# Kernel tuning notes

Measured on AMD Instinct MI355X. Metric: run time of the kernel, lower is better.

The kernel has to match this reference:

```python
import jax, jax.numpy as jnp
import numpy as np

LATENT = 1024
HID = 512
J = 24
# SMPL kinematic tree (parent[0] = -1 is the root, unused in the loop)
PARENT = [-1, 0, 0, 0, 1, 2, 3, 4, 5, 6, 7, 8, 9, 9, 9, 12, 13, 14, 16, 17, 18, 19, 20, 21]
EPS = 1e-12  # F.normalize default eps


def setup_inputs() -> dict:
    key = jax.random.key(0)
    k1, k2, k3, k4, k5 = jax.random.split(key, 5)
    B = 32768
    # Kaiming-uniform-ish init scales for the Linear layers
    s1 = 1.0 / np.sqrt(LATENT)
    s2 = 1.0 / np.sqrt(HID)
    return {
        "z": jax.random.normal(k1, (B, LATENT), dtype=jnp.float32),
        "W1": jax.random.uniform(k2, (LATENT, HID), minval=-s1, maxval=s1, dtype=jnp.float32),
        "b1": jax.random.uniform(k3, (HID,), minval=-s1, maxval=s1, dtype=jnp.float32),
        "W2": jax.random.uniform(k4, (HID, (J - 1) * 4), minval=-s2, maxval=s2, dtype=jnp.float32),
        "b2": jax.random.uniform(k5, ((J - 1) * 4,), minval=-s2, maxval=s2, dtype=jnp.float32),
    }


def reference(z, W1, b1, W2, b2):
    B = z.shape[0]
    h = jax.nn.silu(z @ W1 + b1)                    # [B, 512]
    raw = (h @ W2 + b2).reshape(B, J - 1, 4)        # [B, J-1, 4]
    vec = raw[..., :3]                              # [B, J-1, 3]
    norm = jnp.linalg.norm(vec, axis=-1, keepdims=True)
    direction = vec / jnp.maximum(norm, EPS)        # F.normalize(dim=-1)
    length = jax.nn.softplus(raw[..., 3])           # [B, J-1]
    child_off = direction * length[..., None]       # [B, J-1, 3]
    offsets = jnp.concatenate(
        [jnp.zeros((B, 1, 3), dtype=z.dtype), child_off], axis=1
    )                                                # [B, J, 3]
    # Static-tree forward kinematics: unroll the (small, fixed) joint loop.
    joints_list = [jnp.zeros((B, 3), dtype=z.dtype)]
    for j in range(1, J):
        joints_list.append(joints_list[PARENT[j]] + offsets[:, j])
    joints = jnp.stack(joints_list, axis=1)          # [B, J, 3]
    return (joints, offsets, length)
```

## Files before the change

kernel.cpp:

```cpp
#include <hip/hip_runtime.h>
#include <hip/hip_bf16.h>
#include <stdint.h>

#define BROWS 32768
#define LATENT 1024
#define HID 512

typedef float f32x4 __attribute__((ext_vector_type(4)));
typedef __bf16 bf16x8 __attribute__((ext_vector_type(8)));
typedef unsigned short us8 __attribute__((ext_vector_type(8)));

__device__ __forceinline__ void gload16(const void* g, void* l) {
  __builtin_amdgcn_global_load_lds(
      (__attribute__((address_space(1))) void*)g,
      (__attribute__((address_space(3))) void*)l, 16, 0, 0);
}

__device__ __forceinline__ void split_bf16(float x, unsigned short& hi, unsigned short& lo) {
  __bf16 h = (__bf16)x;
  float r = x - (float)h;
  __bf16 l = (__bf16)r;
  hi = __builtin_bit_cast(unsigned short, h);
  lo = __builtin_bit_cast(unsigned short, l);
}

__device__ __forceinline__ f32x4 mfma16(bf16x8 a, bf16x8 b, f32x4 c) {
  return __builtin_amdgcn_mfma_f32_16x16x32_bf16(a, b, c, 0, 0, 0);
}

__device__ __forceinline__ bf16x8 ldfrag(const void* p) {
  return __builtin_bit_cast(bf16x8, *(const us8*)p);
}

__global__ __launch_bounds__(256) void k_prep_w1f(const float* __restrict__ W1,
                                                  unsigned short* __restrict__ w1f) {
  const int n = blockIdx.x;
  const int t = threadIdx.x;
  const int kt = t >> 3, ls = t & 7;
  const int p = ls ^ (n & 7);
  const int k0 = kt * 32 + (ls & 3) * 8;
  unsigned short v[8];
#pragma unroll
  for (int e = 0; e < 8; e++) {
    const float x = W1[(size_t)(k0 + e) * HID + n];
    unsigned short h, q;
    split_bf16(x, h, q);
    v[e] = (ls < 4) ? h : q;
  }
  unsigned short* dst = w1f + ((size_t)n * 32 + kt) * 64 + p * 8;
  *(ushort4*)(dst) = make_ushort4(v[0], v[1], v[2], v[3]);
  *(ushort4*)(dst + 4) = make_ushort4(v[4], v[5], v[6], v[7]);
}

__global__ __launch_bounds__(256) void k_prep_w2t(const float* __restrict__ W2,
                                                  unsigned short* __restrict__ hi,
                                                  unsigned short* __restrict__ lo) {
  const int idx = blockIdx.x * 256 + threadIdx.x;
  const int n = idx >> 9, k = idx & 511;
  const float v = (n < 92) ? W2[(size_t)k * 92 + n] : 0.0f;
  unsigned short h, l;
  split_bf16(v, h, l);
  hi[idx] = h;
  lo[idx] = l;
}

__global__ __launch_bounds__(256, 2) void k_gemm1(
    const float* __restrict__ z, const unsigned short* __restrict__ w1f,
    const float* __restrict__ b1,
    unsigned short* __restrict__ hh, unsigned short* __restrict__ hl) {
  extern __shared__ __align__(16) char lb[];

  const int tid = threadIdx.x;
  const int bid = blockIdx.x;
  const int swz = (bid & 7) * 64 + (bid >> 3);
  const int mb = swz >> 1, nbk = swz & 1;
  const int m0 = mb * 128, n0g = nbk * 256;

  const int wv = tid >> 6, l = tid & 63;
  const int wr = wv >> 1, wc = wv & 1;
  const int l15 = l & 15, lg = l >> 4;
  const int xr = l15 & 7;

  const int bhB = (wc * 128 + l15) * 128 + ((lg ^ xr) << 4);
  const int blB = (wc * 128 + l15) * 128 + ((((4 | lg) ^ xr)) << 4);

  const float* zb = z + (size_t)(m0 + wr * 64 + l15) * LATENT + lg * 8;

  const unsigned short* bsrc =
      w1f + ((size_t)(n0g + wv * 64 + (l >> 3)) * 32) * 64 + (l & 7) * 8;

  f32x4 acc[4][8] = {};
  float4 arl[4], arh[4];
  bf16x8 ah[4], alo[4];

#define LOAD_A(kt1)                                                           \
  {                                                                           \
    _Pragma("unroll") for (int mf = 0; mf < 4; mf++) {                        \
      const float* p_ = zb + (size_t)(16 * mf) * LATENT + (kt1) * 32;         \
      arl[mf] = *(const float4*)(p_);                                         \
      arh[mf] = *(const float4*)(p_ + 4);                                     \
    }                                                                         \
  }

#define SPLIT_A                                                               \
  {                                                                           \
    _Pragma("unroll") for (int mf = 0; mf < 4; mf++) {                        \
      _Pragma("unroll") for (int e = 0; e < 4; e++) {                         \
        float f0 = arl[mf][e], f1 = arh[mf][e];                               \
        __bf16 h0 = (__bf16)f0, h1 = (__bf16)f1;                              \
        ah[mf][e] = h0;     alo[mf][e] = (__bf16)(f0 - (float)h0);            \
        ah[mf][4 + e] = h1; alo[mf][4 + e] = (__bf16)(f1 - (float)h1);        \
      }                                                                       \
    }                                                                         \
  }

#define GLOAD_B(bufo, kt1)                                                    \
  {                                                                           \
    _Pragma("unroll") for (int j_ = 0; j_ < 8; j_++)                          \
        gload16(bsrc + (size_t)j_ * 16384 + (kt1) * 64,                       \
                lb + (bufo) + (wv * 64 + j_ * 8) * 128);                      \
  }

#define COMPUTE(bufo)                                                         \
  {                                                                           \
    __builtin_amdgcn_s_setprio(1);                                            \
    _Pragma("unroll") for (int nf = 0; nf < 8; nf++) {                        \
      bf16x8 bh = ldfrag(lb + (bufo) + bhB + nf * 2048);                      \
      _Pragma("unroll") for (int mf = 0; mf < 4; mf++)                        \
          acc[mf][nf] = mfma16(ah[mf], bh, acc[mf][nf]);                      \
      _Pragma("unroll") for (int mf = 0; mf < 4; mf++)                        \
          acc[mf][nf] = mfma16(alo[mf], bh, acc[mf][nf]);                     \
    }                                                                         \
    _Pragma("unroll") for (int nf = 0; nf < 8; nf++) {                        \
      bf16x8 bl = ldfrag(lb + (bufo) + blB + nf * 2048);                      \
      _Pragma("unroll") for (int mf = 0; mf < 4; mf++)                        \
          acc[mf][nf] = mfma16(ah[mf], bl, acc[mf][nf]);                      \
    }                                                                         \
    __builtin_amdgcn_s_setprio(0);                                            \
  }

  GLOAD_B(0, 0);
  LOAD_A(0);

#pragma unroll 2
  for (int t = 0; t < 32; ++t) {
    const int cb = (t & 1) * 32768;
    const int nb2 = cb ^ 32768;

    asm volatile("s_waitcnt vmcnt(8)" ::: "memory");
    __builtin_amdgcn_s_barrier();

    if (t < 31) {
      GLOAD_B(nb2, t + 1);
      asm volatile("s_waitcnt vmcnt(8)" ::: "memory");
    } else {
      asm volatile("s_waitcnt vmcnt(0)" ::: "memory");
    }
    SPLIT_A;
    if (t < 31) LOAD_A(t + 1);

    COMPUTE(cb);
  }

  float b1v[8];
#pragma unroll
  for (int nf = 0; nf < 8; nf++) b1v[nf] = b1[n0g + wc * 128 + nf * 16 + l15];

#pragma unroll
  for (int mf = 0; mf < 4; mf++)
#pragma unroll
    for (int nf = 0; nf < 8; nf++)
#pragma unroll
      for (int r = 0; r < 4; r++) {
        const int gm = m0 + wr * 64 + mf * 16 + (lg << 2) + r;
        const int gn = n0g + wc * 128 + nf * 16 + l15;
        const float x = acc[mf][nf][r] + b1v[nf];
        const float hval = x / (1.0f + expf(-x));
        unsigned short hi_, lo_;
        split_bf16(hval, hi_, lo_);
        const size_t o = (size_t)gm * HID + gn;
        hh[o] = hi_;
        hl[o] = lo_;
      }
}

__global__ __launch_bounds__(256, 2) void k_gemm2(
    const unsigned short* __restrict__ hh, const unsigned short* __restrict__ hl,
    const unsigned short* __restrict__ w2h, const unsigned short* __restrict__ w2l,
    const float* __restrict__ b2, float* __restrict__ out) {
  __shared__ unsigned short Ah[2][2048], Al[2][2048];
  __shared__ unsigned short Bh[2][4096], Bl[2][4096];
  __shared__ float raw[64][97];

  const int tid = threadIdx.x;
  const int m0 = blockIdx.x * 64;
  const int w = tid >> 6, lane = tid & 63;
  const int wr = w >> 1, wc = w & 1;
  const int l15 = lane & 15, lg = lane >> 4;
  const int arow = tid >> 2, ac8 = (tid & 3) << 3;

  const unsigned short* hhb = hh + (size_t)(m0 + arow) * HID + ac8;
  const unsigned short* hlb = hl + (size_t)(m0 + arow) * HID + ac8;
  const unsigned short* w2hb = w2h + (size_t)arow * HID + ac8;
  const unsigned short* w2lb = w2l + (size_t)arow * HID + ac8;

  f32x4 acc[2][3] = {};

#define G2_STAGE(kt, bf) { \
    gload16(hhb + (kt) * 32, &Ah[bf][(w << 9)]); \
    gload16(hlb + (kt) * 32, &Al[bf][(w << 9)]); \
    gload16(w2hb + (kt) * 32,            &Bh[bf][(w << 9)]); \
    gload16(w2hb + (kt) * 32 + 64 * HID, &Bh[bf][2048 + (w << 9)]); \
    gload16(w2lb + (kt) * 32,            &Bl[bf][(w << 9)]); \
    gload16(w2lb + (kt) * 32 + 64 * HID, &Bl[bf][2048 + (w << 9)]); }

#define G2_COMPUTE(bf) { \
    bf16x8 ah2[2], al2[2], bh2[3], bl2[3]; \
    _Pragma("unroll") \
    for (int mf = 0; mf < 2; mf++) { \
      const int o_ = ((wr * 32 + mf * 16 + l15) << 5) + (lg << 3); \
      ah2[mf] = ldfrag(&Ah[bf][o_]); \
      al2[mf] = ldfrag(&Al[bf][o_]); \
    } \
    _Pragma("unroll") \
    for (int nf = 0; nf < 3; nf++) { \
      const int o_ = ((wc * 48 + nf * 16 + l15) << 5) + (lg << 3); \
      bh2[nf] = ldfrag(&Bh[bf][o_]); \
      bl2[nf] = ldfrag(&Bl[bf][o_]); \
    } \
    _Pragma("unroll") \
    for (int mf = 0; mf < 2; mf++) { \
      _Pragma("unroll") \
      for (int nf = 0; nf < 3; nf++) { \
        acc[mf][nf] = mfma16(ah2[mf], bh2[nf], acc[mf][nf]); \
        acc[mf][nf] = mfma16(al2[mf], bh2[nf], acc[mf][nf]); \
        acc[mf][nf] = mfma16(ah2[mf], bl2[nf], acc[mf][nf]); \
      } } }

  G2_STAGE(0, 0);
  __syncthreads();
#pragma unroll 2
  for (int kt = 0; kt < 16; kt++) {
    const int cur = kt & 1, nx = cur ^ 1;
    if (kt < 15) G2_STAGE(kt + 1, nx);
    G2_COMPUTE(cur);
    __syncthreads();
  }

#pragma unroll
  for (int mf = 0; mf < 2; mf++) {
#pragma unroll
    for (int nf = 0; nf < 3; nf++) {
#pragma unroll
      for (int r = 0; r < 4; r++) {
        const int ml = wr * 32 + mf * 16 + (lg << 2) + r;
        const int nl = wc * 48 + nf * 16 + l15;
        raw[ml][nl] = acc[mf][nf][r];
      }
    }
  }
  __syncthreads();

  const size_t OFFB = (size_t)BROWS * 72;
  const size_t LENB = (size_t)BROWS * 144;

  for (int task = tid; task < 64 * 24; task += 256) {
    const int row = task / 24;
    const int j = task - row * 24;
    const int gm = m0 + row;
    float* orow = out + OFFB + (size_t)gm * 72;
    if (j == 0) {
      orow[0] = 0.0f; orow[1] = 0.0f; orow[2] = 0.0f;
    } else {
      const int c0 = (j - 1) * 4;
      const float vx = raw[row][c0 + 0] + b2[c0 + 0];
      const float vy = raw[row][c0 + 1] + b2[c0 + 1];
      const float vz = raw[row][c0 + 2] + b2[c0 + 2];
      const float wvv = raw[row][c0 + 3] + b2[c0 + 3];
      const float nrm = sqrtf(vx * vx + vy * vy + vz * vz);
      const float inv = 1.0f / fmaxf(nrm, 1e-12f);
      const float len = fmaxf(wvv, 0.0f) + log1pf(expf(-fabsf(wvv)));
      const float sc = inv * len;
      const float ox = vx * sc, oy = vy * sc, oz = vz * sc;
      orow[j * 3 + 0] = ox; orow[j * 3 + 1] = oy; orow[j * 3 + 2] = oz;
      out[LENB + (size_t)gm * 23 + (j - 1)] = len;
      raw[row][c0 + 0] = ox; raw[row][c0 + 1] = oy; raw[row][c0 + 2] = oz;
    }
  }
  __syncthreads();

  if (tid < 64) {
    constexpr int PAR[24] = {-1, 0, 0, 0, 1, 2, 3, 4, 5, 6, 7, 8,
                             9, 9, 9, 12, 13, 14, 16, 17, 18, 19, 20, 21};
    const int gm = m0 + tid;
    float e[72];
    e[0] = 0.0f; e[1] = 0.0f; e[2] = 0.0f;
#pragma unroll
    for (int j = 1; j < 24; j++) {
      const int p = PAR[j];
      const int c0 = (j - 1) * 4;
      e[3 * j + 0] = e[3 * p + 0] + raw[tid][c0 + 0];
      e[3 * j + 1] = e[3 * p + 1] + raw[tid][c0 + 1];
      e[3 * j + 2] = e[3 * p + 2] + raw[tid][c0 + 2];
    }
    float4* jo = (float4*)(out + (size_t)gm * 72);
#pragma unroll
    for (int q = 0; q < 18; q++)
      jo[q] = make_float4(e[4 * q + 0], e[4 * q + 1], e[4 * q + 2], e[4 * q + 3]);
  }
}

extern "C" void kernel_launch(void* const* d_in, const int* in_sizes, int n_in,
                              void* d_out, int out_size, void* d_ws, size_t ws_size,
                              hipStream_t stream) {
  const float* z = (const float*)d_in[0];
  const float* W1 = (const float*)d_in[1];
  const float* b1 = (const float*)d_in[2];
  const float* W2 = (const float*)d_in[3];
  const float* b2 = (const float*)d_in[4];
  float* out = (float*)d_out;

  char* ws = (char*)d_ws;
  unsigned short* w1f = (unsigned short*)(ws);
  unsigned short* w2h = (unsigned short*)(ws + (2 << 20));
  unsigned short* w2l = (unsigned short*)(ws + (2 << 20) + 131072);
  unsigned short* hh = (unsigned short*)(ws + ((size_t)4 << 20));
  unsigned short* hl = (unsigned short*)(ws + ((size_t)4 << 20) + ((size_t)32 << 20));

  hipFuncSetAttribute((const void*)k_gemm1,
                      hipFuncAttributeMaxDynamicSharedMemorySize, 131072);

  hipLaunchKernelGGL(k_prep_w1f, dim3(512), dim3(256), 0, stream, W1, w1f);
  hipLaunchKernelGGL(k_prep_w2t, dim3(256), dim3(256), 0, stream, W2, w2h, w2l);
  hipLaunchKernelGGL(k_gemm1, dim3(512), dim3(256), 65536, stream, z, w1f, b1, hh, hl);
  hipLaunchKernelGGL(k_gemm2, dim3(512), dim3(256), 0, stream, hh, hl, w2h, w2l, b2, out);
}
```

Before: 147.8 us.

## Shrink GEMM1 to single-wave 64x64 tiles without block barriers

Restructures the first GEMM from 256-thread blocks computing 128x256 tiles into single-wave 64-thread blocks computing 64x64 tiles, launched as 4096 blocks with static 32KB LDS. Because each block is one wave, the workgroup barrier is dropped and only vmcnt waits order the double-buffered LDS loads. The goal is to remove barrier stalls and raise occupancy and scheduling flexibility. The cost is far less reuse: each z row tile is reloaded and re-split by 8 column blocks instead of 2, and each W1 tile is fetched by many more blocks, which raises global and L2 traffic.

```diff
diff --git a/kernel.cpp b/kernel.cpp
--- a/kernel.cpp
+++ b/kernel.cpp
@@ -64,32 +64,30 @@
   lo[idx] = l;
 }
 
-__global__ __launch_bounds__(256, 2) void k_gemm1(
+__global__ __launch_bounds__(64, 3) void k_gemm1(
     const float* __restrict__ z, const unsigned short* __restrict__ w1f,
     const float* __restrict__ b1,
     unsigned short* __restrict__ hh, unsigned short* __restrict__ hl) {
-  extern __shared__ __align__(16) char lb[];
-
-  const int tid = threadIdx.x;
+  __shared__ __attribute__((aligned(16))) char lb[32768];
+
   const int bid = blockIdx.x;
-  const int swz = (bid & 7) * 64 + (bid >> 3);
-  const int mb = swz >> 1, nbk = swz & 1;
-  const int m0 = mb * 128, n0g = nbk * 256;
-
-  const int wv = tid >> 6, l = tid & 63;
-  const int wr = wv >> 1, wc = wv & 1;
+  const int swz = (bid & 7) * 512 + (bid >> 3);
+  const int mb = swz >> 3, nbk = swz & 7;
+  const int m0 = mb * 64, n0g = nbk * 64;
+
+  const int l = threadIdx.x;
   const int l15 = l & 15, lg = l >> 4;
   const int xr = l15 & 7;
 
-  const int bhB = (wc * 128 + l15) * 128 + ((lg ^ xr) << 4);
-  const int blB = (wc * 128 + l15) * 128 + ((((4 | lg) ^ xr)) << 4);
-
-  const float* zb = z + (size_t)(m0 + wr * 64 + l15) * LATENT + lg * 8;
+  const int bhB = l15 * 128 + ((lg ^ xr) << 4);
+  const int blB = l15 * 128 + ((((4 | lg) ^ xr)) << 4);
+
+  const float* zb = z + (size_t)(m0 + l15) * LATENT + lg * 8;
 
   const unsigned short* bsrc =
-      w1f + ((size_t)(n0g + wv * 64 + (l >> 3)) * 32) * 64 + (l & 7) * 8;
-
-  f32x4 acc[4][8] = {};
+      w1f + ((size_t)(n0g + (l >> 3)) * 32) * 64 + (l & 7) * 8;
+
+  f32x4 acc[4][4] = {};
   float4 arl[4], arh[4];
   bf16x8 ah[4], alo[4];
 
@@ -118,20 +116,20 @@
   {                                                                           \
     _Pragma("unroll") for (int j_ = 0; j_ < 8; j_++)                          \
         gload16(bsrc + (size_t)j_ * 16384 + (kt1) * 64,                       \
-                lb + (bufo) + (wv * 64 + j_ * 8) * 128);                      \
+                lb + (bufo) + j_ * 1024);                                     \
   }
 
 #define COMPUTE(bufo)                                                         \
   {                                                                           \
     __builtin_amdgcn_s_setprio(1);                                            \
-    _Pragma("unroll") for (int nf = 0; nf < 8; nf++) {                        \
+    _Pragma("unroll") for (int nf = 0; nf < 4; nf++) {                        \
       bf16x8 bh = ldfrag(lb + (bufo) + bhB + nf * 2048);                      \
       _Pragma("unroll") for (int mf = 0; mf < 4; mf++)                        \
           acc[mf][nf] = mfma16(ah[mf], bh, acc[mf][nf]);                      \
       _Pragma("unroll") for (int mf = 0; mf < 4; mf++)                        \
           acc[mf][nf] = mfma16(alo[mf], bh, acc[mf][nf]);                     \
     }                                                                         \
-    _Pragma("unroll") for (int nf = 0; nf < 8; nf++) {                        \
+    _Pragma("unroll") for (int nf = 0; nf < 4; nf++) {                        \
       bf16x8 bl = ldfrag(lb + (bufo) + blB + nf * 2048);                      \
       _Pragma("unroll") for (int mf = 0; mf < 4; mf++)                        \
           acc[mf][nf] = mfma16(ah[mf], bl, acc[mf][nf]);                      \
@@ -139,41 +137,38 @@
     __builtin_amdgcn_s_setprio(0);                                            \
   }
 
+#define FENCE asm volatile("" ::: "memory")
+
   GLOAD_B(0, 0);
+  FENCE;
   LOAD_A(0);
 
-#pragma unroll 2
   for (int t = 0; t < 32; ++t) {
-    const int cb = (t & 1) * 32768;
-    const int nb2 = cb ^ 32768;
+    const int cb = (t & 1) << 13;
+    const int nx = cb ^ 8192;
 
     asm volatile("s_waitcnt vmcnt(8)" ::: "memory");
-    __builtin_amdgcn_s_barrier();
-
     if (t < 31) {
-      GLOAD_B(nb2, t + 1);
-      asm volatile("s_waitcnt vmcnt(8)" ::: "memory");
-    } else {
-      asm volatile("s_waitcnt vmcnt(0)" ::: "memory");
+      GLOAD_B(nx, t + 1);
+      FENCE;
     }
     SPLIT_A;
     if (t < 31) LOAD_A(t + 1);
-
     COMPUTE(cb);
   }
 
-  float b1v[8];
-#pragma unroll
-  for (int nf = 0; nf < 8; nf++) b1v[nf] = b1[n0g + wc * 128 + nf * 16 + l15];
+  float b1v[4];
+#pragma unroll
+  for (int nf = 0; nf < 4; nf++) b1v[nf] = b1[n0g + nf * 16 + l15];
 
 #pragma unroll
   for (int mf = 0; mf < 4; mf++)
 #pragma unroll
-    for (int nf = 0; nf < 8; nf++)
+    for (int nf = 0; nf < 4; nf++)
 #pragma unroll
       for (int r = 0; r < 4; r++) {
-        const int gm = m0 + wr * 64 + mf * 16 + (lg << 2) + r;
-        const int gn = n0g + wc * 128 + nf * 16 + l15;
+        const int gm = m0 + mf * 16 + (lg << 2) + r;
+        const int gn = n0g + nf * 16 + l15;
         const float x = acc[mf][nf][r] + b1v[nf];
         const float hval = x / (1.0f + expf(-x));
         unsigned short hi_, lo_;
@@ -327,11 +322,8 @@
   unsigned short* hh = (unsigned short*)(ws + ((size_t)4 << 20));
   unsigned short* hl = (unsigned short*)(ws + ((size_t)4 << 20) + ((size_t)32 << 20));
 
-  hipFuncSetAttribute((const void*)k_gemm1,
-                      hipFuncAttributeMaxDynamicSharedMemorySize, 131072);
-
   hipLaunchKernelGGL(k_prep_w1f, dim3(512), dim3(256), 0, stream, W1, w1f);
   hipLaunchKernelGGL(k_prep_w2t, dim3(256), dim3(256), 0, stream, W2, w2h, w2l);
-  hipLaunchKernelGGL(k_gemm1, dim3(512), dim3(256), 65536, stream, z, w1f, b1, hh, hl);
+  hipLaunchKernelGGL(k_gemm1, dim3(4096), dim3(64), 0, stream, z, w1f, b1, hh, hl);
   hipLaunchKernelGGL(k_gemm2, dim3(512), dim3(256), 0, stream, hh, hl, w2h, w2l, b2, out);
 }
```

Result: slower. 244.3 us (+65.2%).

## Restructure GEMM1 to 8 waves with LDS-staged A tiles and phased MFMA pipeline

Applied to the files above, without the earlier changes.

GEMM1 moves from 4 to 8 waves per block, each wave computing a 64x64 sub-tile instead of 64x128. The fp32 z tile is now staged into LDS through async global-to-LDS loads, replacing direct register loads, and shares a double buffer with the B tile. The main loop splits into three MFMA phases (hi*hi, lo*hi, hi*lo) with barriers between them so fragment loads and prefetch can overlap compute. This lowers per-wave register pressure and raises latency hiding, at the cost of more barriers and more LDS (96KB per block), which may limit occupancy.

```diff
diff --git a/kernel.cpp b/kernel.cpp
--- a/kernel.cpp
+++ b/kernel.cpp
@@ -64,7 +64,7 @@
   lo[idx] = l;
 }
 
-__global__ __launch_bounds__(256, 2) void k_gemm1(
+__global__ __launch_bounds__(512, 2) void k_gemm1(
     const float* __restrict__ z, const unsigned short* __restrict__ w1f,
     const float* __restrict__ b1,
     unsigned short* __restrict__ hh, unsigned short* __restrict__ hl) {
@@ -77,103 +77,132 @@
   const int m0 = mb * 128, n0g = nbk * 256;
 
   const int wv = tid >> 6, l = tid & 63;
-  const int wr = wv >> 1, wc = wv & 1;
+  const int wr = wv >> 2, wc = wv & 3;
   const int l15 = l & 15, lg = l >> 4;
-  const int xr = l15 & 7;
-
-  const int bhB = (wc * 128 + l15) * 128 + ((lg ^ xr) << 4);
-  const int blB = (wc * 128 + l15) * 128 + ((((4 | lg) ^ xr)) << 4);
-
-  const float* zb = z + (size_t)(m0 + wr * 64 + l15) * LATENT + lg * 8;
-
-  const unsigned short* bsrc =
-      w1f + ((size_t)(n0g + wv * 64 + (l >> 3)) * 32) * 64 + (l & 7) * 8;
-
-  f32x4 acc[4][8] = {};
-  float4 arl[4], arh[4];
-  bf16x8 ah[4], alo[4];
-
-#define LOAD_A(kt1)                                                           \
+  const int x7 = l15 & 7;
+
+  const int rowAB = (wr * 64 + l15) * 128;
+  const int sA0 = (((2 * lg) ^ x7)) << 4;
+  const int sA1 = (((2 * lg + 1) ^ x7)) << 4;
+  const int rowBB = 16384 + (wc * 64 + l15) * 128;
+  const int sBH = ((lg ^ x7)) << 4;
+  const int sBL = ((((4 | lg)) ^ x7)) << 4;
+
+  const int lr = l >> 3, lc = l & 7;
+  const char* zA0 = (const char*)z +
+      ((size_t)(m0 + wv * 16 + lr)) * 4096 + ((lc ^ (lr & 7)) << 4);
+  const char* zB0 = (const char*)w1f +
+      ((size_t)(n0g + wv * 32 + lr)) * 4096 + (lc << 4);
+
+  f32x4 acc[4][4] = {};
+  f32x4 af[4][2];
+  bf16x8 ah[4], al[4], bhf[4], blf[4];
+
+#define STAGE(nbase, kt1)                                                     \
+  {                                                                           \
+    _Pragma("unroll") for (int j_ = 0; j_ < 2; j_++)                          \
+        gload16(zA0 + (size_t)j_ * 32768 + (kt1) * 128,                       \
+                lb + (nbase) + (wv * 2 + j_) * 1024);                         \
+    _Pragma("unroll") for (int j_ = 0; j_ < 4; j_++)                          \
+        gload16(zB0 + (size_t)j_ * 32768 + (kt1) * 128,                       \
+                lb + (nbase) + 16384 + (wv * 4 + j_) * 1024);                 \
+  }
+
+#define LD_A(cb)                                                              \
   {                                                                           \
     _Pragma("unroll") for (int mf = 0; mf < 4; mf++) {                        \
-      const float* p_ = zb + (size_t)(16 * mf) * LATENT + (kt1) * 32;         \
-      arl[mf] = *(const float4*)(p_);                                         \
-      arh[mf] = *(const float4*)(p_ + 4);                                     \
+      af[mf][0] = *(const f32x4*)(lb + (cb) + rowAB + mf * 2048 + sA0);       \
+      af[mf][1] = *(const f32x4*)(lb + (cb) + rowAB + mf * 2048 + sA1);       \
     }                                                                         \
   }
 
-#define SPLIT_A                                                               \
-  {                                                                           \
-    _Pragma("unroll") for (int mf = 0; mf < 4; mf++) {                        \
-      _Pragma("unroll") for (int e = 0; e < 4; e++) {                         \
-        float f0 = arl[mf][e], f1 = arh[mf][e];                               \
-        __bf16 h0 = (__bf16)f0, h1 = (__bf16)f1;                              \
-        ah[mf][e] = h0;     alo[mf][e] = (__bf16)(f0 - (float)h0);            \
-        ah[mf][4 + e] = h1; alo[mf][4 + e] = (__bf16)(f1 - (float)h1);        \
-      }                                                                       \
+#define LD_BH(cb)                                                             \
+  {                                                                           \
+    _Pragma("unroll") for (int nf = 0; nf < 4; nf++)                          \
+        bhf[nf] = ldfrag(lb + (cb) + rowBB + nf * 2048 + sBH);                \
+  }
+
+#define LD_BL(cb)                                                             \
+  {                                                                           \
+    _Pragma("unroll") for (int nf = 0; nf < 4; nf++)                          \
+        blf[nf] = ldfrag(lb + (cb) + rowBB + nf * 2048 + sBL);                \
+  }
+
+#define SPLIT_HI                                                              \
+  {                                                                           \
+    _Pragma("unroll") for (int mf = 0; mf < 4; mf++)                          \
+        _Pragma("unroll") for (int e = 0; e < 4; e++) {                       \
+      ah[mf][e] = (__bf16)af[mf][0][e];                                       \
+      ah[mf][4 + e] = (__bf16)af[mf][1][e];                                   \
     }                                                                         \
   }
 
-#define GLOAD_B(bufo, kt1)                                                    \
-  {                                                                           \
-    _Pragma("unroll") for (int j_ = 0; j_ < 8; j_++)                          \
-        gload16(bsrc + (size_t)j_ * 16384 + (kt1) * 64,                       \
-                lb + (bufo) + (wv * 64 + j_ * 8) * 128);                      \
-  }
-
-#define COMPUTE(bufo)                                                         \
+#define SPLIT_LO                                                              \
+  {                                                                           \
+    _Pragma("unroll") for (int mf = 0; mf < 4; mf++)                          \
+        _Pragma("unroll") for (int e = 0; e < 4; e++) {                       \
+      al[mf][e] = (__bf16)(af[mf][0][e] - (float)ah[mf][e]);                  \
+      al[mf][4 + e] = (__bf16)(af[mf][1][e] - (float)ah[mf][4 + e]);          \
+    }                                                                         \
+  }
+
+#define MCL(AF, BF)                                                           \
   {                                                                           \
     __builtin_amdgcn_s_setprio(1);                                            \
-    _Pragma("unroll") for (int nf = 0; nf < 8; nf++) {                        \
-      bf16x8 bh = ldfrag(lb + (bufo) + bhB + nf * 2048);                      \
-      _Pragma("unroll") for (int mf = 0; mf < 4; mf++)                        \
-          acc[mf][nf] = mfma16(ah[mf], bh, acc[mf][nf]);                      \
-      _Pragma("unroll") for (int mf = 0; mf < 4; mf++)                        \
-          acc[mf][nf] = mfma16(alo[mf], bh, acc[mf][nf]);                     \
-    }                                                                         \
-    _Pragma("unroll") for (int nf = 0; nf < 8; nf++) {                        \
-      bf16x8 bl = ldfrag(lb + (bufo) + blB + nf * 2048);                      \
-      _Pragma("unroll") for (int mf = 0; mf < 4; mf++)                        \
-          acc[mf][nf] = mfma16(ah[mf], bl, acc[mf][nf]);                      \
-    }                                                                         \
+    _Pragma("unroll") for (int mf = 0; mf < 4; mf++)                          \
+        _Pragma("unroll") for (int nf = 0; nf < 4; nf++)                      \
+            acc[mf][nf] = mfma16(AF[mf], BF[nf], acc[mf][nf]);                \
     __builtin_amdgcn_s_setprio(0);                                            \
   }
 
-  GLOAD_B(0, 0);
-  LOAD_A(0);
+#define SBAR { asm volatile("" ::: "memory"); __builtin_amdgcn_s_barrier();   \
+               asm volatile("" ::: "memory"); }
+#define VM0  asm volatile("s_waitcnt vmcnt(0)" ::: "memory")
+
+  STAGE(0, 0);
+  VM0;
+  SBAR;
+  LD_A(0);
+  LD_BH(0);
 
 #pragma unroll 2
   for (int t = 0; t < 32; ++t) {
-    const int cb = (t & 1) * 32768;
-    const int nb2 = cb ^ 32768;
-
-    asm volatile("s_waitcnt vmcnt(8)" ::: "memory");
-    __builtin_amdgcn_s_barrier();
-
-    if (t < 31) {
-      GLOAD_B(nb2, t + 1);
-      asm volatile("s_waitcnt vmcnt(8)" ::: "memory");
-    } else {
-      asm volatile("s_waitcnt vmcnt(0)" ::: "memory");
+    const int cb = (t & 1) * 49152;
+    const int nb = cb ^ 49152;
+    const bool pre = (t < 31);
+
+    LD_BL(cb);
+    if (pre) STAGE(nb, t + 1);
+    SBAR;
+    SPLIT_HI;
+    MCL(ah, bhf);
+    SBAR;
+
+    SPLIT_LO;
+    MCL(al, bhf);
+
+    VM0;
+    SBAR;
+    MCL(ah, blf);
+    if (pre) {
+      LD_A(nb);
+      LD_BH(nb);
     }
-    SPLIT_A;
-    if (t < 31) LOAD_A(t + 1);
-
-    COMPUTE(cb);
-  }
-
-  float b1v[8];
-#pragma unroll
-  for (int nf = 0; nf < 8; nf++) b1v[nf] = b1[n0g + wc * 128 + nf * 16 + l15];
+    SBAR;
+  }
+
+  float b1v[4];
+#pragma unroll
+  for (int nf = 0; nf < 4; nf++) b1v[nf] = b1[n0g + wc * 64 + nf * 16 + l15];
 
 #pragma unroll
   for (int mf = 0; mf < 4; mf++)
 #pragma unroll
-    for (int nf = 0; nf < 8; nf++)
+    for (int nf = 0; nf < 4; nf++)
 #pragma unroll
       for (int r = 0; r < 4; r++) {
         const int gm = m0 + wr * 64 + mf * 16 + (lg << 2) + r;
-        const int gn = n0g + wc * 128 + nf * 16 + l15;
+        const int gn = n0g + wc * 64 + nf * 16 + l15;
         const float x = acc[mf][nf][r] + b1v[nf];
         const float hval = x / (1.0f + expf(-x));
         unsigned short hi_, lo_;
@@ -328,10 +357,10 @@
   unsigned short* hl = (unsigned short*)(ws + ((size_t)4 << 20) + ((size_t)32 << 20));
 
   hipFuncSetAttribute((const void*)k_gemm1,
-                      hipFuncAttributeMaxDynamicSharedMemorySize, 131072);
+                      hipFuncAttributeMaxDynamicSharedMemorySize, 98304);
 
   hipLaunchKernelGGL(k_prep_w1f, dim3(512), dim3(256), 0, stream, W1, w1f);
   hipLaunchKernelGGL(k_prep_w2t, dim3(256), dim3(256), 0, stream, W2, w2h, w2l);
-  hipLaunchKernelGGL(k_gemm1, dim3(512), dim3(256), 65536, stream, z, w1f, b1, hh, hl);
+  hipLaunchKernelGGL(k_gemm1, dim3(512), dim3(512), 98304, stream, z, w1f, b1, hh, hl);
   hipLaunchKernelGGL(k_gemm2, dim3(512), dim3(256), 0, stream, hh, hl, w2h, w2l, b2, out);
 }
```

Measured after the change: 157.1 us. 6.3% more time.
